# Optimization experiments

Hardware: AMD Instinct MI355X
Metric: run time of the kernel (lower is better)

The kernel has to match this reference:

```python
import jax, jax.numpy as jnp
import numpy as np

DIM = 512
NUM_HEADS = 16
HEAD_DIM = DIM // NUM_HEADS
RES = (32, 32)
SEQ_SCALE = float(np.log(RES[0] * RES[1]))  # seq_length_scale buffer
TABLE = (2 * RES[0] - 1) * (2 * RES[1] - 1)  # 3969
EPS = 1e-12


def setup_inputs() -> dict:
    key = jax.random.key(0)
    ks = jax.random.split(key, 12)
    B, N, C = 8, RES[0] * RES[1], DIM
    s = 0.02
    return {
        "x": jax.random.normal(ks[0], (B, N, C), dtype=jnp.float32),
        "_h": RES[0],
        "_w": RES[1],
        "relative_pos_index": jax.random.randint(ks[1], (N, N), 0, TABLE, dtype=jnp.int32),
        "relative_coords_table": jax.random.uniform(ks[2], (TABLE, 2), dtype=jnp.float32, minval=-1.0, maxval=1.0),
        "qkv_w": jax.random.normal(ks[3], (3 * C, C), dtype=jnp.float32) * s,
        "qkv_b": jnp.zeros((3 * C,), dtype=jnp.float32),
        "proj_w": jax.random.normal(ks[4], (C, C), dtype=jnp.float32) * s,
        "proj_b": jnp.zeros((C,), dtype=jnp.float32),
        "temperature": jnp.full((NUM_HEADS, 1, 1), float(np.log(np.expm1(1.0 / 0.24))), dtype=jnp.float32),
        "query_embedding": jax.random.normal(ks[5], (NUM_HEADS, 1, HEAD_DIM), dtype=jnp.float32) * s,
        "cpb_fc1_w": jax.random.normal(ks[6], (512, 2), dtype=jnp.float32) * s,
        "cpb_fc1_b": jnp.zeros((512,), dtype=jnp.float32),
        "cpb_fc2_w": jax.random.normal(ks[7], (NUM_HEADS, 512), dtype=jnp.float32) * s,
        "cpb_fc2_b": jnp.zeros((NUM_HEADS,), dtype=jnp.float32),
    }


def _l2norm(t):
    # F.normalize(t, dim=-1): x / max(||x||, eps)
    n = jnp.sqrt(jnp.sum(t * t, axis=-1, keepdims=True))
    return t / jnp.maximum(n, EPS)


def reference(x, _h, _w, relative_pos_index, relative_coords_table,
              qkv_w, qkv_b, proj_w, proj_b, temperature, query_embedding,
              cpb_fc1_w, cpb_fc1_b, cpb_fc2_w, cpb_fc2_b):
    B, N, C = x.shape
    H, hd = NUM_HEADS, HEAD_DIM
    # qkv projection -> [B, N, 3H, hd] -> [B, 3H, N, hd]
    qkv = (x @ qkv_w.T + qkv_b).reshape(B, N, 3 * H, hd).transpose(0, 2, 1, 3)
    q, k, v = jnp.split(qkv, 3, axis=1)  # each [B, H, N, hd]
    # CPB MLP relative bias: [T,2] -> [T,H] -> gather -> [H,N,N]
    t = jax.nn.relu(relative_coords_table @ cpb_fc1_w.T + cpb_fc1_b) @ cpb_fc2_w.T + cpb_fc2_b
    rel_bias = t[relative_pos_index].transpose(2, 0, 1)  # [H, N, N]
    # cosine attention with learned softplus temperature and query embedding
    scale = jax.nn.softplus(temperature) * SEQ_SCALE  # [H,1,1]
    qn = (_l2norm(q) + query_embedding[None]) * scale[None]
    kn = _l2norm(k)
    attn = jnp.einsum('bhnd,bhmd->bhnm', qn, kn) + rel_bias[None]
    attn = jax.nn.softmax(attn, axis=-1)
    out = jnp.einsum('bhnm,bhmd->bhnd', attn, v)  # [B,H,N,hd]
    out = out.transpose(0, 2, 1, 3).reshape(B, N, C)
    return out @ proj_w.T + proj_b
```

## Files before the change

kernel.cpp:

```cpp
#include <hip/hip_runtime.h>
#include <cstdint>
#include <cstddef>

typedef _Float16 f16;
typedef _Float16 f16x4 __attribute__((ext_vector_type(4)));
typedef _Float16 f16x8 __attribute__((ext_vector_type(8)));
typedef float f32x4 __attribute__((ext_vector_type(4)));

#define MFMA32(a,b,c) __builtin_amdgcn_mfma_f32_16x16x32_f16((a),(b),(c),0,0,0)
#define MFMA16(a,b,c) __builtin_amdgcn_mfma_f32_16x16x16f16((a),(b),(c),0,0,0)

__device__ __forceinline__ void gload_lds16(const f16* g, f16* l) {
  __builtin_amdgcn_global_load_lds(
      (const __attribute__((address_space(1))) unsigned int*)g,
      (__attribute__((address_space(3))) unsigned int*)l, 16, 0, 0);
}

static constexpr size_t OFF_TCPB = 0;
static constexpr size_t OFF_BIAS = 262144;
static constexpr size_t OFF_XHI  = OFF_BIAS + 33554432;
static constexpr size_t OFF_XLO  = OFF_XHI + 8388608;
static constexpr size_t OFF_WHI  = OFF_XLO + 8388608;
static constexpr size_t OFF_WLO  = OFF_WHI + 1572864;
static constexpr size_t OFF_PW   = OFF_WLO + 1572864;
static constexpr size_t OFF_QHI  = OFF_PW  + 524288;
static constexpr size_t OFF_QLO  = OFF_QHI + 8388608;
static constexpr size_t OFF_KHI  = OFF_QLO + 8388608;
static constexpr size_t OFF_KLO  = OFF_KHI + 8388608;
static constexpr size_t OFF_VT   = OFF_KLO + 8388608;
static constexpr size_t OFF_AO   = OFF_VT  + 8388608;

__global__ __launch_bounds__(256) void k_convert(
    const float* __restrict__ x, const float* __restrict__ qw, const float* __restrict__ pwf,
    f16* __restrict__ xhi, f16* __restrict__ xlo,
    f16* __restrict__ whi, f16* __restrict__ wlo, f16* __restrict__ pw)
{
  int i = blockIdx.x * 256 + threadIdx.x;
  const float4* src; f16* dh; f16* dl; int j;
  if (i < 1048576)      { j = i;           src = (const float4*)x;   dh = xhi; dl = xlo; }
  else if (i < 1245184) { j = i - 1048576; src = (const float4*)qw;  dh = whi; dl = wlo; }
  else                  { j = i - 1245184; src = (const float4*)pwf; dh = pw;  dl = nullptr; }
  float4 v = src[j];
  f16x4 h;
  h[0] = (f16)v.x; h[1] = (f16)v.y; h[2] = (f16)v.z; h[3] = (f16)v.w;
  ((f16x4*)dh)[j] = h;
  if (dl) {
    f16x4 l;
    l[0] = (f16)(v.x - (float)h[0]); l[1] = (f16)(v.y - (float)h[1]);
    l[2] = (f16)(v.z - (float)h[2]); l[3] = (f16)(v.w - (float)h[3]);
    ((f16x4*)dl)[j] = l;
  }
}

__global__ __launch_bounds__(64) void k_cpb(
    const float* __restrict__ table, const float* __restrict__ w1, const float* __restrict__ b1,
    const float* __restrict__ w2, const float* __restrict__ b2, float* __restrict__ t_out)
{
  const int r = blockIdx.x;
  const int lane = threadIdx.x;
  const float c0 = table[2*r], c1 = table[2*r+1];
  const int j0 = lane * 8;
  float h[8];
#pragma unroll
  for (int jj = 0; jj < 8; jj++) {
    int j = j0 + jj;
    float v = c0 * w1[2*j] + c1 * w1[2*j+1] + b1[j];
    h[jj] = v > 0.0f ? v : 0.0f;
  }
  float acc[16];
#pragma unroll
  for (int o = 0; o < 16; o++) {
    const float4* wp = (const float4*)(w2 + o*512 + j0);
    float4 a = wp[0], bb = wp[1];
    acc[o] = a.x*h[0] + a.y*h[1] + a.z*h[2] + a.w*h[3]
           + bb.x*h[4] + bb.y*h[5] + bb.z*h[6] + bb.w*h[7];
  }
#pragma unroll
  for (int o = 0; o < 16; o++) {
    float v = acc[o];
    for (int s = 1; s < 64; s <<= 1) v += __shfl_xor(v, s, 64);
    acc[o] = v;
  }
  if (lane == 0) {
#pragma unroll
    for (int o = 0; o < 16; o++) t_out[r*16 + o] = acc[o] + b2[o];
  }
}

__global__ __launch_bounds__(256) void k_bias(
    const int* __restrict__ idx, const float* __restrict__ t_cpb, f16* __restrict__ bias_t)
{
  const int m4 = blockIdx.x >> 6, ng = blockIdx.x & 63;
  const int h = threadIdx.x >> 4, nl = threadIdx.x & 15;
  const int n = ng*16 + nl;
  int4 I = *(const int4*)(idx + (size_t)n*1024 + m4*4);
  f16x4 o;
  o[0] = (f16)t_cpb[I.x*16 + h];
  o[1] = (f16)t_cpb[I.y*16 + h];
  o[2] = (f16)t_cpb[I.z*16 + h];
  o[3] = (f16)t_cpb[I.w*16 + h];
  *(f16x4*)(bias_t + (((size_t)h*256 + m4)*1024 + n)*4) = o;
}

__global__ __launch_bounds__(256) void k_qkv(
    const f16* __restrict__ xhi, const f16* __restrict__ xlo,
    const f16* __restrict__ whi, const f16* __restrict__ wlo,
    const float* __restrict__ qkvb, const float* __restrict__ temp, const float* __restrict__ qe,
    f16* __restrict__ qh_o, f16* __restrict__ ql_o,
    f16* __restrict__ kh_o, f16* __restrict__ vt_o)
{
  __shared__ __align__(16) f16 Ah[8][64][8];
  __shared__ __align__(16) f16 Al[8][64][8];
  __shared__ __align__(16) f16 Bh[8][64][8];
  __shared__ __align__(16) f16 Bl[8][64][8];
  const int tid = threadIdx.x, lane = tid & 63, w = tid >> 6;
  const int rsel = lane & 15, ksel = lane >> 4;
  const int bx = blockIdx.x & 63, by = blockIdx.x >> 6;
  const int m0 = bx << 7, n0 = by << 7;
  const bool SPLIT = (by < 8);

  const size_t aoff = (size_t)(m0 + w*32 + rsel)*512 + ksel*8;
  const size_t boff = (size_t)(n0 + w*32 + rsel)*512 + ksel*8;
  const f16 *gA0 = xhi + aoff,  *gA1 = gA0 + 16*512;
  const f16 *gAl0 = xlo + aoff, *gAl1 = gAl0 + 16*512;
  const f16 *gB0 = whi + boff,  *gB1 = gB0 + 16*512;
  const f16 *gBl0 = wlo + boff, *gBl1 = gBl0 + 16*512;
  f16 *lA0 = &Ah[2*w][0][0],  *lA1 = &Ah[2*w+1][0][0];
  f16 *lAl0 = &Al[2*w][0][0], *lAl1 = &Al[2*w+1][0][0];
  f16 *lB0 = &Bh[2*w][0][0],  *lB1 = &Bh[2*w+1][0][0];
  f16 *lBl0 = &Bl[2*w][0][0], *lBl1 = &Bl[2*w+1][0][0];

  const f32x4 zero = {0.f, 0.f, 0.f, 0.f};
  f32x4 acc[4][4];
#pragma unroll
  for (int mt = 0; mt < 4; mt++)
#pragma unroll
    for (int nt = 0; nt < 4; nt++) acc[mt][nt] = zero;

  const int mb4 = (w & 1) * 4, nb4 = (w >> 1) * 4;
  for (int k0 = 0; k0 < 512; k0 += 32) {
    __syncthreads();
    gload_lds16(gA0 + k0, lA0);
    gload_lds16(gA1 + k0, lA1);
    gload_lds16(gB0 + k0, lB0);
    gload_lds16(gB1 + k0, lB1);
    if (SPLIT) {
      gload_lds16(gAl0 + k0, lAl0);
      gload_lds16(gAl1 + k0, lAl1);
      gload_lds16(gBl0 + k0, lBl0);
      gload_lds16(gBl1 + k0, lBl1);
    }
    __syncthreads();
    f16x8 bhf[4], blf[4];
#pragma unroll
    for (int nt = 0; nt < 4; nt++) bhf[nt] = ((const f16x8*)&Bh[nb4+nt][0][0])[lane];
    if (SPLIT) {
#pragma unroll
      for (int nt = 0; nt < 4; nt++) blf[nt] = ((const f16x8*)&Bl[nb4+nt][0][0])[lane];
#pragma unroll
      for (int mt = 0; mt < 4; mt++) {
        f16x8 ah = ((const f16x8*)&Ah[mb4+mt][0][0])[lane];
        f16x8 al = ((const f16x8*)&Al[mb4+mt][0][0])[lane];
#pragma unroll
        for (int nt = 0; nt < 4; nt++) {
          acc[mt][nt] = MFMA32(al, bhf[nt], acc[mt][nt]);
          acc[mt][nt] = MFMA32(ah, blf[nt], acc[mt][nt]);
          acc[mt][nt] = MFMA32(ah, bhf[nt], acc[mt][nt]);
        }
      }
    } else {
#pragma unroll
      for (int mt = 0; mt < 4; mt++) {
        f16x8 ah = ((const f16x8*)&Ah[mb4+mt][0][0])[lane];
#pragma unroll
        for (int nt = 0; nt < 4; nt++)
          acc[mt][nt] = MFMA32(ah, bhf[nt], acc[mt][nt]);
      }
    }
  }

  const int mbase = m0 + (w & 1)*64, nbase = n0 + (w >> 1)*64;
  float bc[4];
#pragma unroll
  for (int nt = 0; nt < 4; nt++) bc[nt] = qkvb[nbase + nt*16 + rsel];
#pragma unroll
  for (int mt = 0; mt < 4; mt++)
#pragma unroll
    for (int nt = 0; nt < 4; nt++)
#pragma unroll
      for (int r = 0; r < 4; r++) acc[mt][nt][r] += bc[nt];

  if (by < 8) {
    const bool ISQ = (by < 4);
#pragma unroll
    for (int pair = 0; pair < 2; pair++) {
      const int h = ((nbase - (ISQ ? 0 : 512)) >> 5) + pair;
      float sc = 0.f, qe0 = 0.f, qe1 = 0.f;
      if (ISQ) {
        sc  = log1pf(__expf(temp[h])) * 6.93147180559945f;
        qe0 = qe[h*32 + rsel];
        qe1 = qe[h*32 + 16 + rsel];
      }
      f16* dh = ISQ ? qh_o : kh_o;
#pragma unroll
      for (int mt = 0; mt < 4; mt++) {
        float ss[4];
#pragma unroll
        for (int r = 0; r < 4; r++) {
          float a = acc[mt][2*pair][r], b = acc[mt][2*pair+1][r];
          ss[r] = a*a + b*b;
        }
        for (int s = 1; s < 16; s <<= 1) {
#pragma unroll
          for (int r = 0; r < 4; r++) ss[r] += __shfl_xor(ss[r], s, 64);
        }
#pragma unroll
        for (int r = 0; r < 4; r++) {
          float rn = 1.0f / fmaxf(sqrtf(ss[r]), 1e-12f);
          int m = mbase + mt*16 + ksel*4 + r;
          int b_ = m >> 10, p = m & 1023;
          size_t base = ((size_t)(b_*16 + h)*1024 + p)*32;
          float v0 = acc[mt][2*pair][r] * rn;
          float v1 = acc[mt][2*pair+1][r] * rn;
          if (ISQ) { v0 = (v0 + qe0) * sc; v1 = (v1 + qe1) * sc; }
          f16 h0 = (f16)v0, h1 = (f16)v1;
          dh[base + rsel]      = h0;
          dh[base + 16 + rsel] = h1;
          if (ISQ) {
            ql_o[base + rsel]      = (f16)(v0 - (float)h0);
            ql_o[base + 16 + rsel] = (f16)(v1 - (float)h1);
          }
        }
      }
    }
  } else {
#pragma unroll
    for (int mt = 0; mt < 4; mt++) {
      int m = mbase + mt*16 + ksel*4;
      int b_ = m >> 10, p = m & 1023;
#pragma unroll
      for (int nt = 0; nt < 4; nt++) {
        int n = nbase + nt*16 + rsel;
        int g = (n - 1024) >> 5, d = n & 31;
        f16x4 pk;
#pragma unroll
        for (int r = 0; r < 4; r++) pk[r] = (f16)acc[mt][nt][r];
        *(f16x4*)(vt_o + ((size_t)(b_*16 + g)*32 + d)*1024 + p) = pk;
      }
    }
  }
}

__global__ __launch_bounds__(256, 4) void k_attn(
    const f16* __restrict__ qhi, const f16* __restrict__ qlo,
    const f16* __restrict__ khi, const f16* __restrict__ vt,
    const f16* __restrict__ bias_t, f16* __restrict__ attnout)
{
  __shared__ __align__(16) f16 OT[4][32][40];
  const int lane = threadIdx.x & 63, w = threadIdx.x >> 6;
  const int rsel = lane & 15, ksel = lane >> 4;
  const int bid = blockIdx.x;
  const int qt = bid & 7, bh = bid >> 3;
  const int h = bh & 15, b = bh >> 4;
  const int q0 = qt*128 + w*32;

  f16x8 Qh[2], Ql[2];
#pragma unroll
  for (int c = 0; c < 2; c++) {
    size_t o = ((size_t)bh*1024 + q0 + c*16 + rsel)*32 + ksel*8;
    Qh[c] = *(const f16x8*)(qhi + o);
    Ql[c] = *(const f16x8*)(qlo + o);
  }
  const f16* kh_base = khi + (size_t)bh*32768;
  const f16* vt_base = vt  + (size_t)bh*32768;
  const f16* bias_h  = bias_t + (size_t)h*1048576;

  const f32x4 zero = {0.f, 0.f, 0.f, 0.f};
  f32x4 O[2][2];
  float mi[2], li[2];
#pragma unroll
  for (int c = 0; c < 2; c++) {
    O[c][0] = zero; O[c][1] = zero;
    mi[c] = -3.0e38f; li[c] = 0.f;
  }

  f16x8 Kh[2];
  Kh[0] = *(const f16x8*)(kh_base + (size_t)(rsel)*32 + ksel*8);
  Kh[1] = *(const f16x8*)(kh_base + (size_t)(16 + rsel)*32 + ksel*8);

  for (int m0 = 0; m0 < 1024; m0 += 32) {
    f16x4 Va[2][2], Bb[2][2];
#pragma unroll
    for (int f = 0; f < 2; f++)
#pragma unroll
      for (int dt = 0; dt < 2; dt++)
        Va[f][dt] = *(const f16x4*)(vt_base + (size_t)(dt*16 + rsel)*1024 + m0 + f*16 + ksel*4);
#pragma unroll
    for (int f = 0; f < 2; f++)
#pragma unroll
      for (int c = 0; c < 2; c++)
        Bb[f][c] = *(const f16x4*)(bias_h + (((size_t)(m0 >> 2) + f*4 + ksel)*1024 + q0 + c*16 + rsel)*4);

    f16x8 Kc0 = Kh[0], Kc1 = Kh[1];
    if (m0 < 992) {
      Kh[0] = *(const f16x8*)(kh_base + (size_t)(m0 + 32 + rsel)*32 + ksel*8);
      Kh[1] = *(const f16x8*)(kh_base + (size_t)(m0 + 48 + rsel)*32 + ksel*8);
    }

    f32x4 St[2][2];
#pragma unroll
    for (int c = 0; c < 2; c++) {
      St[0][c] = MFMA32(Kc0, Ql[c], zero);
      St[0][c] = MFMA32(Kc0, Qh[c], St[0][c]);
      St[1][c] = MFMA32(Kc1, Ql[c], zero);
      St[1][c] = MFMA32(Kc1, Qh[c], St[1][c]);
    }

    f16x4 P16[2][2];
#pragma unroll
    for (int c = 0; c < 2; c++) {
      float s[8];
#pragma unroll
      for (int f = 0; f < 2; f++)
#pragma unroll
        for (int r = 0; r < 4; r++) s[f*4+r] = St[f][c][r] + (float)Bb[f][c][r];
      float cm = s[0];
#pragma unroll
      for (int i = 1; i < 8; i++) cm = fmaxf(cm, s[i]);
      cm = fmaxf(cm, __shfl_xor(cm, 16, 64));
      cm = fmaxf(cm, __shfl_xor(cm, 32, 64));
      float mn = fmaxf(mi[c], cm);
      float alpha = __expf(mi[c] - mn);
      mi[c] = mn;
      float p[8], rs = 0.f;
#pragma unroll
      for (int i = 0; i < 8; i++) { p[i] = __expf(s[i] - mn); rs += p[i]; }
      rs += __shfl_xor(rs, 16, 64);
      rs += __shfl_xor(rs, 32, 64);
      li[c] = li[c]*alpha + rs;
#pragma unroll
      for (int dt = 0; dt < 2; dt++)
#pragma unroll
        for (int r = 0; r < 4; r++) O[c][dt][r] *= alpha;
#pragma unroll
      for (int f = 0; f < 2; f++)
#pragma unroll
        for (int r = 0; r < 4; r++) P16[f][c][r] = (f16)p[f*4+r];
    }
#pragma unroll
    for (int c = 0; c < 2; c++)
#pragma unroll
      for (int dt = 0; dt < 2; dt++) {
        O[c][dt] = MFMA16(Va[0][dt], P16[0][c], O[c][dt]);
        O[c][dt] = MFMA16(Va[1][dt], P16[1][c], O[c][dt]);
      }
  }

#pragma unroll
  for (int c = 0; c < 2; c++) {
    float inv = 1.0f / li[c];
#pragma unroll
    for (int dt = 0; dt < 2; dt++)
#pragma unroll
      for (int r = 0; r < 4; r++)
        OT[w][c*16 + rsel][dt*16 + ksel*4 + r] = (f16)(O[c][dt][r] * inv);
  }
  int row = lane >> 1, half = lane & 1;
  f16x8 o0 = *(const f16x8*)(&OT[w][row][half*16]);
  f16x8 o1 = *(const f16x8*)(&OT[w][row][half*16 + 8]);
  f16* outp = attnout + ((size_t)b*1024 + q0 + row)*512 + h*32 + half*16;
  *(f16x8*)outp = o0;
  *(f16x8*)(outp + 8) = o1;
}

__global__ __launch_bounds__(256) void k_proj(
    const f16* __restrict__ A, const f16* __restrict__ Bw,
    const float* __restrict__ pb, float* __restrict__ out)
{
  __shared__ __align__(16) f16 Ah[8][64][8];
  __shared__ __align__(16) f16 Bh[8][64][8];
  const int tid = threadIdx.x, lane = tid & 63, w = tid >> 6;
  const int rsel = lane & 15, ksel = lane >> 4;
  const int bx = blockIdx.x & 63, by = blockIdx.x >> 6;
  const int m0 = bx << 7, n0 = by << 7;
  const f16 *gA0 = A + (size_t)(m0 + w*32 + rsel)*512 + ksel*8,  *gA1 = gA0 + 16*512;
  const f16 *gB0 = Bw + (size_t)(n0 + w*32 + rsel)*512 + ksel*8, *gB1 = gB0 + 16*512;
  f16 *lA0 = &Ah[2*w][0][0], *lA1 = &Ah[2*w+1][0][0];
  f16 *lB0 = &Bh[2*w][0][0], *lB1 = &Bh[2*w+1][0][0];
  const f32x4 zero = {0.f, 0.f, 0.f, 0.f};
  f32x4 acc[4][4];
#pragma unroll
  for (int mt = 0; mt < 4; mt++)
#pragma unroll
    for (int nt = 0; nt < 4; nt++) acc[mt][nt] = zero;
  const int mb4 = (w & 1)*4, nb4 = (w >> 1)*4;
  for (int k0 = 0; k0 < 512; k0 += 32) {
    __syncthreads();
    gload_lds16(gA0 + k0, lA0);
    gload_lds16(gA1 + k0, lA1);
    gload_lds16(gB0 + k0, lB0);
    gload_lds16(gB1 + k0, lB1);
    __syncthreads();
    f16x8 bhf[4];
#pragma unroll
    for (int nt = 0; nt < 4; nt++) bhf[nt] = ((const f16x8*)&Bh[nb4+nt][0][0])[lane];
#pragma unroll
    for (int mt = 0; mt < 4; mt++) {
      f16x8 ah = ((const f16x8*)&Ah[mb4+mt][0][0])[lane];
#pragma unroll
      for (int nt = 0; nt < 4; nt++)
        acc[mt][nt] = MFMA32(ah, bhf[nt], acc[mt][nt]);
    }
  }
  const int mbase = m0 + (w & 1)*64, nbase = n0 + (w >> 1)*64;
  float bc[4];
#pragma unroll
  for (int nt = 0; nt < 4; nt++) bc[nt] = pb[nbase + nt*16 + rsel];
#pragma unroll
  for (int mt = 0; mt < 4; mt++)
#pragma unroll
    for (int nt = 0; nt < 4; nt++)
#pragma unroll
      for (int r = 0; r < 4; r++)
        out[(size_t)(mbase + mt*16 + ksel*4 + r)*512 + nbase + nt*16 + rsel] =
            acc[mt][nt][r] + bc[nt];
}

extern "C" void kernel_launch(void* const* d_in, const int* in_sizes, int n_in,
                              void* d_out, int out_size, void* d_ws, size_t ws_size,
                              hipStream_t stream) {
  const float* x    = (const float*)d_in[0];
  const int*   rpi  = (const int*)d_in[3];
  const float* rct  = (const float*)d_in[4];
  const float* qw   = (const float*)d_in[5];
  const float* qb   = (const float*)d_in[6];
  const float* pwf  = (const float*)d_in[7];
  const float* pbv  = (const float*)d_in[8];
  const float* temp = (const float*)d_in[9];
  const float* qe   = (const float*)d_in[10];
  const float* f1w  = (const float*)d_in[11];
  const float* f1b  = (const float*)d_in[12];
  const float* f2w  = (const float*)d_in[13];
  const float* f2b  = (const float*)d_in[14];

  char* ws = (char*)d_ws;
  float* t_cpb  = (float*)(ws + OFF_TCPB);
  f16* bias_t   = (f16*)(ws + OFF_BIAS);
  f16* xhi = (f16*)(ws + OFF_XHI);
  f16* xlo = (f16*)(ws + OFF_XLO);
  f16* whi = (f16*)(ws + OFF_WHI);
  f16* wlo = (f16*)(ws + OFF_WLO);
  f16* pw  = (f16*)(ws + OFF_PW);
  f16* qhi = (f16*)(ws + OFF_QHI);
  f16* qlo = (f16*)(ws + OFF_QLO);
  f16* khi = (f16*)(ws + OFF_KHI);
  f16* vt  = (f16*)(ws + OFF_VT);
  f16* ao  = (f16*)(ws + OFF_AO);

  k_convert<<<5120, 256, 0, stream>>>(x, qw, pwf, xhi, xlo, whi, wlo, pw);
  k_cpb<<<3969, 64, 0, stream>>>(rct, f1w, f1b, f2w, f2b, t_cpb);
  k_bias<<<16384, 256, 0, stream>>>(rpi, t_cpb, bias_t);
  k_qkv<<<768, 256, 0, stream>>>(xhi, xlo, whi, wlo, qb, temp, qe,
                                 qhi, qlo, khi, vt);
  k_attn<<<1024, 256, 0, stream>>>(qhi, qlo, khi, vt, bias_t, ao);
  k_proj<<<256, 256, 0, stream>>>(ao, pw, pbv, (float*)d_out);
}
```

Measured before the change: 302.6 us.

## Split attention over key range and merge partial softmax results

The attention kernel now splits the 1024-key range into two halves per block, doubling the grid to 2048 blocks and raising the occupancy hint. Each half writes a normalized partial output plus its running max and sum, and a new merge kernel combines them with softmax rescaling into the layout the projection expects. The row-sum cross-lane reduction is deferred to the end of the loop, and the CPB kernel packs four table rows per 256-thread block. This adds an extra kernel launch and extra global traffic for the partial outputs, and reuses workspace regions (xhi/xlo/klo) that must no longer be live at that point.

```diff
diff --git a/kernel.cpp b/kernel.cpp
--- a/kernel.cpp
+++ b/kernel.cpp
@@ -52,12 +52,13 @@
   }
 }
 
-__global__ __launch_bounds__(64) void k_cpb(
+__global__ __launch_bounds__(256) void k_cpb(
     const float* __restrict__ table, const float* __restrict__ w1, const float* __restrict__ b1,
     const float* __restrict__ w2, const float* __restrict__ b2, float* __restrict__ t_out)
 {
-  const int r = blockIdx.x;
-  const int lane = threadIdx.x;
+  const int r = blockIdx.x * 4 + (threadIdx.x >> 6);
+  const int lane = threadIdx.x & 63;
+  if (r >= 3969) return;
   const float c0 = table[2*r], c1 = table[2*r+1];
   const int j0 = lane * 8;
   float h[8];
@@ -251,18 +252,21 @@
   }
 }
 
-__global__ __launch_bounds__(256, 4) void k_attn(
+__global__ __launch_bounds__(256, 8) void k_attn(
     const f16* __restrict__ qhi, const f16* __restrict__ qlo,
     const f16* __restrict__ khi, const f16* __restrict__ vt,
-    const f16* __restrict__ bias_t, f16* __restrict__ attnout)
+    const f16* __restrict__ bias_t,
+    f16* __restrict__ po0, f16* __restrict__ po1,
+    float2* __restrict__ ml0, float2* __restrict__ ml1)
 {
   __shared__ __align__(16) f16 OT[4][32][40];
   const int lane = threadIdx.x & 63, w = threadIdx.x >> 6;
   const int rsel = lane & 15, ksel = lane >> 4;
   const int bid = blockIdx.x;
-  const int qt = bid & 7, bh = bid >> 3;
-  const int h = bh & 15, b = bh >> 4;
+  const int qt = bid & 7, split = (bid >> 3) & 1, bh = bid >> 4;
+  const int h = bh & 15;
   const int q0 = qt*128 + w*32;
+  const int mstart = split * 512;
 
   f16x8 Qh[2], Ql[2];
 #pragma unroll
@@ -285,10 +289,10 @@
   }
 
   f16x8 Kh[2];
-  Kh[0] = *(const f16x8*)(kh_base + (size_t)(rsel)*32 + ksel*8);
-  Kh[1] = *(const f16x8*)(kh_base + (size_t)(16 + rsel)*32 + ksel*8);
-
-  for (int m0 = 0; m0 < 1024; m0 += 32) {
+  Kh[0] = *(const f16x8*)(kh_base + (size_t)(mstart + rsel)*32 + ksel*8);
+  Kh[1] = *(const f16x8*)(kh_base + (size_t)(mstart + 16 + rsel)*32 + ksel*8);
+
+  for (int m0 = mstart; m0 < mstart + 512; m0 += 32) {
     f16x4 Va[2][2], Bb[2][2];
 #pragma unroll
     for (int f = 0; f < 2; f++)
@@ -302,7 +306,7 @@
         Bb[f][c] = *(const f16x4*)(bias_h + (((size_t)(m0 >> 2) + f*4 + ksel)*1024 + q0 + c*16 + rsel)*4);
 
     f16x8 Kc0 = Kh[0], Kc1 = Kh[1];
-    if (m0 < 992) {
+    if (m0 < mstart + 480) {
       Kh[0] = *(const f16x8*)(kh_base + (size_t)(m0 + 32 + rsel)*32 + ksel*8);
       Kh[1] = *(const f16x8*)(kh_base + (size_t)(m0 + 48 + rsel)*32 + ksel*8);
     }
@@ -335,8 +339,6 @@
       float p[8], rs = 0.f;
 #pragma unroll
       for (int i = 0; i < 8; i++) { p[i] = __expf(s[i] - mn); rs += p[i]; }
-      rs += __shfl_xor(rs, 16, 64);
-      rs += __shfl_xor(rs, 32, 64);
       li[c] = li[c]*alpha + rs;
 #pragma unroll
       for (int dt = 0; dt < 2; dt++)
@@ -358,6 +360,8 @@
 
 #pragma unroll
   for (int c = 0; c < 2; c++) {
+    li[c] += __shfl_xor(li[c], 16, 64);
+    li[c] += __shfl_xor(li[c], 32, 64);
     float inv = 1.0f / li[c];
 #pragma unroll
     for (int dt = 0; dt < 2; dt++)
@@ -365,12 +369,48 @@
       for (int r = 0; r < 4; r++)
         OT[w][c*16 + rsel][dt*16 + ksel*4 + r] = (f16)(O[c][dt][r] * inv);
   }
+  f16* po_s = split ? po1 : po0;
+  float2* ml_s = split ? ml1 : ml0;
   int row = lane >> 1, half = lane & 1;
   f16x8 o0 = *(const f16x8*)(&OT[w][row][half*16]);
   f16x8 o1 = *(const f16x8*)(&OT[w][row][half*16 + 8]);
-  f16* outp = attnout + ((size_t)b*1024 + q0 + row)*512 + h*32 + half*16;
+  f16* outp = po_s + ((size_t)bh*1024 + q0 + row)*32 + half*16;
   *(f16x8*)outp = o0;
   *(f16x8*)(outp + 8) = o1;
+  if (lane < 32) {
+    int c = lane >> 4;
+    float mm = c ? mi[1] : mi[0];
+    float ll = c ? li[1] : li[0];
+    ml_s[(size_t)bh*1024 + q0 + lane] = make_float2(mm, ll);
+  }
+}
+
+__global__ __launch_bounds__(256) void k_merge(
+    const f16* __restrict__ po0, const f16* __restrict__ po1,
+    const float2* __restrict__ ml0, const float2* __restrict__ ml1,
+    f16* __restrict__ ao)
+{
+  int tid = blockIdx.x * 256 + threadIdx.x;
+  int h = tid & 15, q = (tid >> 4) & 1023, b = tid >> 14;
+  int bh = b*16 + h;
+  size_t rec = (size_t)bh*1024 + q;
+  float2 a = ml0[rec], c = ml1[rec];
+  float M = fmaxf(a.x, c.x);
+  float w0 = a.y * __expf(a.x - M);
+  float w1 = c.y * __expf(c.x - M);
+  float inv = 1.0f / (w0 + w1);
+  w0 *= inv; w1 *= inv;
+  const f16x8* p0 = (const f16x8*)(po0 + rec*32);
+  const f16x8* p1 = (const f16x8*)(po1 + rec*32);
+  f16* op = ao + ((size_t)b*1024 + q)*512 + h*32;
+#pragma unroll
+  for (int i = 0; i < 4; i++) {
+    f16x8 x0 = p0[i], x1 = p1[i];
+    f16x8 o;
+#pragma unroll
+    for (int j = 0; j < 8; j++) o[j] = (f16)((float)x0[j]*w0 + (float)x1[j]*w1);
+    ((f16x8*)op)[i] = o;
+  }
 }
 
 __global__ __launch_bounds__(256) void k_proj(
@@ -456,12 +496,17 @@
   f16* khi = (f16*)(ws + OFF_KHI);
   f16* vt  = (f16*)(ws + OFF_VT);
   f16* ao  = (f16*)(ws + OFF_AO);
+  f16* po0 = (f16*)(ws + OFF_KLO);
+  f16* po1 = (f16*)(ws + OFF_XHI);
+  float2* ml0 = (float2*)(ws + OFF_XLO);
+  float2* ml1 = ml0 + 131072;
 
   k_convert<<<5120, 256, 0, stream>>>(x, qw, pwf, xhi, xlo, whi, wlo, pw);
-  k_cpb<<<3969, 64, 0, stream>>>(rct, f1w, f1b, f2w, f2b, t_cpb);
+  k_cpb<<<993, 256, 0, stream>>>(rct, f1w, f1b, f2w, f2b, t_cpb);
   k_bias<<<16384, 256, 0, stream>>>(rpi, t_cpb, bias_t);
   k_qkv<<<768, 256, 0, stream>>>(xhi, xlo, whi, wlo, qb, temp, qe,
                                  qhi, qlo, khi, vt);
-  k_attn<<<1024, 256, 0, stream>>>(qhi, qlo, khi, vt, bias_t, ao);
+  k_attn<<<2048, 256, 0, stream>>>(qhi, qlo, khi, vt, bias_t, po0, po1, ml0, ml1);
+  k_merge<<<512, 256, 0, stream>>>(po0, po1, ml0, ml1, ao);
   k_proj<<<256, 256, 0, stream>>>(ao, pw, pbv, (float*)d_out);
 }
```

Result: slower. 599.6 us (+98.1%).
